# Performance work log

Hardware: AMD Instinct MI355X
Metric: run time of the kernel (lower is better)

Reference implementation:

```python
import jax, jax.numpy as jnp
import numpy as np

N, M, DIM, HEADS = 32768, 2048, 128, 8
TAU = 0.1


def setup_inputs() -> dict:
    key = jax.random.key(0)
    ks = jax.random.split(key, 7)
    return {
        "x1": jax.random.normal(ks[0], (N, DIM), jnp.float32),
        "k": jax.random.normal(ks[1], (N, DIM), jnp.float32),
        "c": jax.random.normal(ks[2], (M, DIM), jnp.float32),
        "Wq": jax.random.normal(ks[3], (DIM * HEADS, DIM), jnp.float32) * 0.02,
        "bq": jax.random.normal(ks[4], (DIM * HEADS,), jnp.float32) * 0.02,
        "Wd": jax.random.normal(ks[5], (DIM, DIM), jnp.float32) * 0.02,
        "bd": jax.random.normal(ks[6], (DIM,), jnp.float32) * 0.02,
    }


def reference(x1, k, c, Wq, bq, Wd, bd):
    # q and k both go through the same 'query' projection (as in the source)
    q = x1 @ Wq.T + bq                      # [N, dim*H]
    kq = k @ Wq.T + bq                      # [N, dim*H]
    C = jnp.tile(c, (1, HEADS))             # torch.cat([c]*H, dim=1) -> [M, dim*H]
    t = q + kq                              # additive attention 'scores' input
    logits = (t @ C.T) / jnp.sqrt(jnp.asarray(DIM, t.dtype))  # [N, M]
    p = jax.nn.softmax(logits, axis=-1)
    # gumbel_softmax(p, tau=0.1, hard=True): -log(Exp(1)) ~ Gumbel(0,1)
    noise = jax.random.gumbel(jax.random.key(42), p.shape, p.dtype)
    y_soft = jax.nn.softmax((p + noise) / TAU, axis=-1)
    idx = jnp.argmax(y_soft, axis=-1)
    y_hard = jax.nn.one_hot(idx, M, dtype=p.dtype)
    y = y_hard - jax.lax.stop_gradient(y_soft) + y_soft  # straight-through
    # attention_dropout and dropout are rate 0.0 -> identity
    out = y.T @ x1                          # [M, dim]
    return out @ Wd.T + bd                  # dense
```

## Files before the change

### kernel.cpp

```cpp
#include <hip/hip_runtime.h>
#include <stdint.h>
#include <math.h>

#define NROW 32768
#define MCOL 2048
#define KDIM 128
#define NHEAD 8
#define SCALE 0.08838834764831845f

typedef __attribute__((ext_vector_type(8))) short short8;
typedef __attribute__((ext_vector_type(4))) float f32x4;

__device__ __forceinline__ uint32_t rotl32(uint32_t x, uint32_t r) {
  return __builtin_amdgcn_alignbit(x, x, 32u - r);
}

__device__ __forceinline__ uint32_t tf_hash(uint32_t c) {
  const uint32_t K2 = 0x1BD11BDAu ^ 0u ^ 42u;
  uint32_t x0 = 0u, x1 = c + 42u;
#define R4A { x0 += x1; x1 = rotl32(x1,13); x1 ^= x0; \
              x0 += x1; x1 = rotl32(x1,15); x1 ^= x0; \
              x0 += x1; x1 = rotl32(x1,26); x1 ^= x0; \
              x0 += x1; x1 = rotl32(x1, 6); x1 ^= x0; }
#define R4B { x0 += x1; x1 = rotl32(x1,17); x1 ^= x0; \
              x0 += x1; x1 = rotl32(x1,29); x1 ^= x0; \
              x0 += x1; x1 = rotl32(x1,16); x1 ^= x0; \
              x0 += x1; x1 = rotl32(x1,24); x1 ^= x0; }
  R4A x0 += 42u;      x1 += K2 + 1u;
  R4B x0 += K2;       x1 += 2u;
  R4A    x1 += 42u + 3u;
  R4B x0 += 42u;      x1 += K2 + 4u;
  R4A x0 += K2;       x1 += 5u;
#undef R4A
#undef R4B
  return x0 ^ x1;
}

__device__ __forceinline__ float bits_to_u(uint32_t b) {
  uint32_t fb = (b >> 9) | 0x3F800000u;
  float f = __uint_as_float(fb) - 1.0f;
  return (f == 0.0f) ? 1.17549435e-38f : f;
}

__device__ __forceinline__ float gumbel_of_key(uint32_t key) {
  float u = bits_to_u(key);
  return -logf(-logf(u));
}

__global__ void k_wsum(const float* __restrict__ Wq, const float* __restrict__ bq,
                       float* __restrict__ Wsum, float* __restrict__ bsum) {
  int t = blockIdx.x * 256 + threadIdx.x;
  if (t < KDIM * KDIM) {
    int d = t >> 7, e = t & 127;
    float s = 0.f;
#pragma unroll
    for (int h = 0; h < NHEAD; ++h) s += Wq[(h * KDIM + d) * KDIM + e];
    Wsum[t] = s;
  }
  if (blockIdx.x == 0 && threadIdx.x < KDIM) {
    int d = threadIdx.x;
    float s = 0.f;
#pragma unroll
    for (int h = 0; h < NHEAD; ++h) s += bq[h * KDIM + d];
    bsum[d] = 2.0f * s;
  }
}

__global__ void k_cw(const float* __restrict__ c, const float* __restrict__ Wsum,
                     const float* __restrict__ bsum,
                     float* __restrict__ cw_s, unsigned short* __restrict__ cwB16,
                     float* __restrict__ cb_s) {
  int m = blockIdx.x;
  int e = threadIdx.x;
  __shared__ float crow[KDIM];
  if (e < 32) ((float4*)crow)[e] = ((const float4*)(c + (size_t)m * KDIM))[e];
  __syncthreads();
  float s = 0.f;
#pragma unroll 4
  for (int d = 0; d < KDIM; ++d) s += crow[d] * Wsum[d * KDIM + e];
  float sv = s * SCALE;
  cw_s[(size_t)m * KDIM + e] = sv;
  {
    int t = m >> 4, col = m & 15, ks = e >> 5, grp = (e >> 3) & 3, j = e & 7;
    int lane = grp * 16 + col;
    cwB16[(((size_t)(t * 4 + ks)) * 64 + lane) * 8 + j] =
        (unsigned short)(__float_as_uint(sv) >> 16);
  }
  if (e == 0) {
    float sb = 0.f;
    for (int d = 0; d < KDIM; ++d) sb += bsum[d] * crow[d];
    cb_s[m] = sb * SCALE;
  }
}

__launch_bounds__(256, 4)
__global__ void k_mega(const float* __restrict__ x1, const float* __restrict__ kin,
                       const uint4* __restrict__ cwB, const float* __restrict__ cb_s,
                       const float* __restrict__ cw_s, float* __restrict__ accum) {
  __shared__ float smx[32];
  __shared__ float sD[32];
  __shared__ float xksh[4][KDIM];

  const int tid = threadIdx.x;
  const int wv = tid >> 6, lane = tid & 63;
  const int B = blockIdx.x * 32;
  const int sstart = wv * 8;

  if (wv < 2) {
    const int R = B + wv * 16;
    const int rowA = R + (lane & 15);
    const int kbase = (lane >> 4) * 8;

    union { uint32_t u[4]; short8 s; } af[4];
#pragma unroll
    for (int ks = 0; ks < 4; ++ks) {
      const float* xp = x1 + (size_t)rowA * KDIM + ks * 32 + kbase;
      const float* kp = kin + (size_t)rowA * KDIM + ks * 32 + kbase;
      float4 a0 = *(const float4*)xp, a1 = *(const float4*)(xp + 4);
      float4 b0 = *(const float4*)kp, b1 = *(const float4*)(kp + 4);
      float f[8] = {a0.x + b0.x, a0.y + b0.y, a0.z + b0.z, a0.w + b0.w,
                    a1.x + b1.x, a1.y + b1.y, a1.z + b1.z, a1.w + b1.w};
#pragma unroll
      for (int r = 0; r < 4; ++r)
        af[ks].u[r] = (__float_as_uint(f[2 * r]) >> 16) |
                      (__float_as_uint(f[2 * r + 1]) & 0xFFFF0000u);
    }

    float mxs[4], Ds[4];
#pragma unroll
    for (int r = 0; r < 4; ++r) { mxs[r] = -INFINITY; Ds[r] = 0.f; }

#pragma unroll 2
    for (int t = 0; t < 128; ++t) {
      f32x4 acc = {0.f, 0.f, 0.f, 0.f};
#pragma unroll
      for (int ks = 0; ks < 4; ++ks) {
        union { uint4 v; short8 s; } bf;
        bf.v = cwB[(size_t)(t * 4 + ks) * 64 + lane];
        acc = __builtin_amdgcn_mfma_f32_16x16x32_bf16(af[ks].s, bf.s, acc, 0, 0, 0);
      }
      float cbv = cb_s[t * 16 + (lane & 15)];
#pragma unroll
      for (int r = 0; r < 4; ++r) {
        float lv = acc[r] + cbv;
        mxs[r] = fmaxf(mxs[r], lv);
        Ds[r] += __expf(lv);
      }
    }

#pragma unroll
    for (int s = 1; s < 16; s <<= 1) {
#pragma unroll
      for (int r = 0; r < 4; ++r) {
        mxs[r] = fmaxf(mxs[r], __shfl_xor(mxs[r], s));
        Ds[r] += __shfl_xor(Ds[r], s);
      }
    }
    if ((lane & 15) == 0) {
#pragma unroll
      for (int r = 0; r < 4; ++r) {
        int lr = wv * 16 + (lane >> 4) * 4 + r;
        smx[lr] = mxs[r];
        sD[lr] = Ds[r];
      }
    }
  }

  uint32_t tk0[8], tk1[8], tk2[8];
#pragma unroll
  for (int ri = 0; ri < 8; ++ri) {
    const int n = B + sstart + ri;
    const uint32_t c0 = (uint32_t)n * (uint32_t)MCOL + (uint32_t)lane;
    uint32_t t0 = 0u, t1 = 0u, t2 = 0u;
#pragma unroll 8
    for (uint32_t jj = 0; jj < 32; ++jj) {
      uint32_t b = tf_hash(c0 + 64u * jj);
      uint32_t key = (b & 0xFFFFFE00u) | jj;
      t2 = max(t2, min(min(t0, t1), key));
      t1 = max(t1, min(t0, key));
      t0 = max(t0, key);
    }
    tk0[ri] = t0; tk1[ri] = t1; tk2[ri] = t2;
  }

  __syncthreads();

#pragma unroll 1
  for (int ri = 0; ri < 8; ++ri) {
    const int n = B + sstart + ri;
    const int lr = sstart + ri;

    uint32_t t0 = tk0[ri], t1 = tk1[ri], t2 = tk2[ri];
    uint32_t kmax = t0;
#pragma unroll
    for (int s = 1; s < 64; s <<= 1)
      kmax = max(kmax, (uint32_t)__shfl_xor((int)kmax, s));

    const float mx = smx[lr], Dp = sD[lr];
    const float pmax = __expf(mx) / Dp;
    const float gstar = gumbel_of_key(kmax);
    const float thr = gstar - (pmax * 1.05f + 2e-4f);

    const float2 xa = ((const float2*)(x1 + (size_t)n * KDIM))[lane];
    const float2 xb = ((const float2*)(kin + (size_t)n * KDIM))[lane];
    const float xk0 = xa.x + xb.x, xk1 = xa.y + xb.y;

    float bestSc = -INFINITY;
    int bestM = 0x7FFFFFFF;

    if (pmax > 0.2f) {
      xksh[wv][lane * 2] = xk0;
      xksh[wv][lane * 2 + 1] = xk1;
      __builtin_amdgcn_s_waitcnt(0);
      for (uint32_t jj = 0; jj < 32; ++jj) {
        uint32_t m = (uint32_t)lane | (jj << 6);
        uint32_t b = tf_hash((uint32_t)n * (uint32_t)MCOL + m);
        float g = -logf(-logf(bits_to_u(b)));
        float l = 0.f;
        for (int e = 0; e < KDIM; ++e) l += xksh[wv][e] * cw_s[(size_t)m * KDIM + e];
        float p = __expf(l + cb_s[m]) / Dp;
        float sc = p + g;
        if (sc > bestSc || (sc == bestSc && (int)m < bestM)) { bestSc = sc; bestM = (int)m; }
      }
#pragma unroll
      for (int s = 1; s < 64; s <<= 1) {
        float os = __shfl_xor(bestSc, s);
        int om = __shfl_xor(bestM, s);
        if (os > bestSc || (os == bestSc && om < bestM)) { bestSc = os; bestM = om; }
      }
    } else {
#pragma unroll
      for (int s = 0; s < 3; ++s) {
        uint32_t tkv = (s == 0) ? t0 : ((s == 1) ? t1 : t2);
        float g = gumbel_of_key(tkv);
        unsigned long long bl = __ballot(g >= thr);
        while (bl) {
          int src = __ffsll(bl) - 1;
          bl &= bl - 1ull;
          uint32_t kk = (uint32_t)__shfl((int)tkv, src);
          float gc = __shfl(g, src);
          int m = src | (int)((kk & 31u) << 6);
          const float2 cv = ((const float2*)(cw_s + (size_t)m * KDIM))[lane];
          float part = xk0 * cv.x + xk1 * cv.y;
#pragma unroll
          for (int sh = 1; sh < 64; sh <<= 1) part += __shfl_xor(part, sh);
          float p = __expf(part + cb_s[m]) / Dp;
          float sc = p + gc;
          if (sc > bestSc || (sc == bestSc && m < bestM)) { bestSc = sc; bestM = m; }
        }
      }
    }

    float* dst = accum + (size_t)bestM * KDIM + lane * 2;
    atomicAdd(dst + 0, xa.x);
    atomicAdd(dst + 1, xa.y);
  }
}

__global__ void k_final(const float* __restrict__ acc, const float* __restrict__ Wd,
                        const float* __restrict__ bd, float* __restrict__ out) {
  int m = blockIdx.x, j = threadIdx.x;
  __shared__ float ar[KDIM];
  if (j < 32) ((float4*)ar)[j] = ((const float4*)(acc + (size_t)m * KDIM))[j];
  __syncthreads();
  const float4* wr = (const float4*)(Wd + (size_t)j * KDIM);
  float s = 0.f;
#pragma unroll
  for (int e4 = 0; e4 < 32; ++e4) {
    float4 wv = wr[e4];
    s += wv.x * ar[4 * e4 + 0] + wv.y * ar[4 * e4 + 1]
       + wv.z * ar[4 * e4 + 2] + wv.w * ar[4 * e4 + 3];
  }
  out[(size_t)m * KDIM + j] = s + bd[j];
}

extern "C" void kernel_launch(void* const* d_in, const int* in_sizes, int n_in,
                              void* d_out, int out_size, void* d_ws, size_t ws_size,
                              hipStream_t stream) {
  const float* x1 = (const float*)d_in[0];
  const float* k  = (const float*)d_in[1];
  const float* c  = (const float*)d_in[2];
  const float* Wq = (const float*)d_in[3];
  const float* bq = (const float*)d_in[4];
  const float* Wd = (const float*)d_in[5];
  const float* bd = (const float*)d_in[6];
  float* out = (float*)d_out;

  char* ws = (char*)d_ws;
  size_t off = 0;
  float* cw_s = (float*)(ws + off); off += (size_t)MCOL * KDIM * 4;
  float* cb_s = (float*)(ws + off); off += 8192;
  unsigned short* cwB = (unsigned short*)(ws + off); off += (size_t)MCOL * KDIM * 2;
  float* Wsum = (float*)(ws + off); off += KDIM * KDIM * 4;
  float* bsum = (float*)(ws + off); off += 4096;
  float* accum = (float*)(ws + off); off += (size_t)MCOL * KDIM * 4;

  hipMemsetAsync(accum, 0, (size_t)MCOL * KDIM * sizeof(float), stream);
  k_wsum<<<64, 256, 0, stream>>>(Wq, bq, Wsum, bsum);
  k_cw<<<MCOL, 128, 0, stream>>>(c, Wsum, bsum, cw_s, cwB, cb_s);
  k_mega<<<1024, 256, 0, stream>>>(x1, k, (const uint4*)cwB, cb_s, cw_s, accum);
  k_final<<<MCOL, 128, 0, stream>>>(accum, Wd, bd, out);
}
```

Baseline: 204.6 us.

## Collect high-Gumbel candidates via ballot compaction and rebalance rows across waves

Drops the per-lane top-3 key tracking. The kernel now compacts every hash above a fixed Gumbel threshold into a per-row shared-memory candidate list using a ballot and prefix popcount. The fast path then scans only those candidates, and it is proven safe when the threshold Gumbel lies below the best candidate minus the probability margin. Otherwise it falls back to the full scan. Rows are split 7/7/9/9 so the MFMA waves do less hashing, and the accum memset is folded into k_wsum. The tradeoff is extra shared memory and ballot traffic in the hash loop, plus a possible rise in fallbacks if candidate counts overflow or the threshold check fails.

```diff
diff --git a/kernel.cpp b/kernel.cpp
--- a/kernel.cpp
+++ b/kernel.cpp
@@ -7,6 +7,7 @@
 #define KDIM 128
 #define NHEAD 8
 #define SCALE 0.08838834764831845f
+#define CSLOTS 24
 
 typedef __attribute__((ext_vector_type(8))) short short8;
 typedef __attribute__((ext_vector_type(4))) float f32x4;
@@ -48,7 +49,8 @@
 }
 
 __global__ void k_wsum(const float* __restrict__ Wq, const float* __restrict__ bq,
-                       float* __restrict__ Wsum, float* __restrict__ bsum) {
+                       float* __restrict__ Wsum, float* __restrict__ bsum,
+                       float* __restrict__ accum) {
   int t = blockIdx.x * 256 + threadIdx.x;
   if (t < KDIM * KDIM) {
     int d = t >> 7, e = t & 127;
@@ -56,6 +58,12 @@
 #pragma unroll
     for (int h = 0; h < NHEAD; ++h) s += Wq[(h * KDIM + d) * KDIM + e];
     Wsum[t] = s;
+  }
+  {
+    float4 z = {0.f, 0.f, 0.f, 0.f};
+    float4* a4 = (float4*)accum;
+#pragma unroll
+    for (int r = 0; r < 4; ++r) a4[t + r * 16384] = z;
   }
   if (blockIdx.x == 0 && threadIdx.x < KDIM) {
     int d = threadIdx.x;
@@ -99,12 +107,17 @@
                        const float* __restrict__ cw_s, float* __restrict__ accum) {
   __shared__ float smx[32];
   __shared__ float sD[32];
+  __shared__ uint2 cls[4][9][CSLOTS];
   __shared__ float xksh[4][KDIM];
 
   const int tid = threadIdx.x;
   const int wv = tid >> 6, lane = tid & 63;
   const int B = blockIdx.x * 32;
-  const int sstart = wv * 8;
+  const int sstart = (wv < 2) ? wv * 7 : 14 + (wv - 2) * 9;
+  const int scnt = (wv < 2) ? 7 : 9;
+
+  const uint32_t BTHR = (__float_as_uint(1.0f + 0.996f) & 0x007FFFFFu) << 9;
+  const float GT = gumbel_of_key(BTHR);
 
   if (wv < 2) {
     const int R = B + wv * 16;
@@ -166,40 +179,40 @@
     }
   }
 
-  uint32_t tk0[8], tk1[8], tk2[8];
-#pragma unroll
-  for (int ri = 0; ri < 8; ++ri) {
-    const int n = B + sstart + ri;
-    const uint32_t c0 = (uint32_t)n * (uint32_t)MCOL + (uint32_t)lane;
-    uint32_t t0 = 0u, t1 = 0u, t2 = 0u;
+  uint32_t rcnt[9];
+#pragma unroll
+  for (int ri = 0; ri < 9; ++ri) {
+    if (ri < scnt) {
+      const int n = B + sstart + ri;
+      const uint32_t c0 = (uint32_t)n * (uint32_t)MCOL + (uint32_t)lane;
+      uint32_t cnt = 0u;
 #pragma unroll 8
-    for (uint32_t jj = 0; jj < 32; ++jj) {
-      uint32_t b = tf_hash(c0 + 64u * jj);
-      uint32_t key = (b & 0xFFFFFE00u) | jj;
-      t2 = max(t2, min(min(t0, t1), key));
-      t1 = max(t1, min(t0, key));
-      t0 = max(t0, key);
-    }
-    tk0[ri] = t0; tk1[ri] = t1; tk2[ri] = t2;
+      for (uint32_t jj = 0; jj < 32; ++jj) {
+        uint32_t b = tf_hash(c0 + 64u * jj);
+        unsigned long long mk = __ballot(b >= BTHR);
+        if (mk) {
+          uint32_t pos = cnt + (uint32_t)__popcll(mk & ((1ull << lane) - 1ull));
+          if (b >= BTHR && pos < CSLOTS)
+            cls[wv][ri][pos] = make_uint2(b, (uint32_t)lane | (jj << 6));
+          cnt += (uint32_t)__popcll(mk);
+        }
+      }
+      rcnt[ri] = cnt;
+    }
   }
 
   __syncthreads();
 
 #pragma unroll 1
-  for (int ri = 0; ri < 8; ++ri) {
-    const int n = B + sstart + ri;
+  for (int ri = 0; ri < 9; ++ri) {
+    if (ri >= scnt) break;
     const int lr = sstart + ri;
-
-    uint32_t t0 = tk0[ri], t1 = tk1[ri], t2 = tk2[ri];
-    uint32_t kmax = t0;
-#pragma unroll
-    for (int s = 1; s < 64; s <<= 1)
-      kmax = max(kmax, (uint32_t)__shfl_xor((int)kmax, s));
+    const int n = B + lr;
+    const uint32_t cnt = rcnt[ri];
 
     const float mx = smx[lr], Dp = sD[lr];
     const float pmax = __expf(mx) / Dp;
-    const float gstar = gumbel_of_key(kmax);
-    const float thr = gstar - (pmax * 1.05f + 2e-4f);
+    const float delta = pmax * 1.05f + 2e-4f;
 
     const float2 xa = ((const float2*)(x1 + (size_t)n * KDIM))[lane];
     const float2 xb = ((const float2*)(kin + (size_t)n * KDIM))[lane];
@@ -208,7 +221,18 @@
     float bestSc = -INFINITY;
     int bestM = 0x7FFFFFFF;
 
-    if (pmax > 0.2f) {
+    uint2 cd = make_uint2(0u, 0u);
+    if (lane < cnt && lane < CSLOTS) cd = cls[wv][ri][lane];
+    uint32_t kmax = cd.x;
+#pragma unroll
+    for (int s = 1; s < 64; s <<= 1)
+      kmax = max(kmax, (uint32_t)__shfl_xor((int)kmax, s));
+    const float gstar = gumbel_of_key(kmax);
+
+    const bool safe = (cnt >= 1u) && (cnt <= CSLOTS) && (pmax <= 0.2f) &&
+                      (GT <= gstar - delta);
+
+    if (!safe) {
       xksh[wv][lane * 2] = xk0;
       xksh[wv][lane * 2 + 1] = xk1;
       __builtin_amdgcn_s_waitcnt(0);
@@ -229,25 +253,21 @@
         if (os > bestSc || (os == bestSc && om < bestM)) { bestSc = os; bestM = om; }
       }
     } else {
-#pragma unroll
-      for (int s = 0; s < 3; ++s) {
-        uint32_t tkv = (s == 0) ? t0 : ((s == 1) ? t1 : t2);
-        float g = gumbel_of_key(tkv);
-        unsigned long long bl = __ballot(g >= thr);
-        while (bl) {
-          int src = __ffsll(bl) - 1;
-          bl &= bl - 1ull;
-          uint32_t kk = (uint32_t)__shfl((int)tkv, src);
-          float gc = __shfl(g, src);
-          int m = src | (int)((kk & 31u) << 6);
-          const float2 cv = ((const float2*)(cw_s + (size_t)m * KDIM))[lane];
-          float part = xk0 * cv.x + xk1 * cv.y;
-#pragma unroll
-          for (int sh = 1; sh < 64; sh <<= 1) part += __shfl_xor(part, sh);
-          float p = __expf(part + cb_s[m]) / Dp;
-          float sc = p + gc;
-          if (sc > bestSc || (sc == bestSc && m < bestM)) { bestSc = sc; bestM = m; }
-        }
+      float g = (lane < cnt) ? gumbel_of_key(cd.x) : -INFINITY;
+      const float thr = gstar - delta;
+      unsigned long long bl = __ballot(g >= thr);
+      while (bl) {
+        int src = __ffsll(bl) - 1;
+        bl &= bl - 1ull;
+        int m = __shfl((int)cd.y, src);
+        float gc = __shfl(g, src);
+        const float2 cv = ((const float2*)(cw_s + (size_t)m * KDIM))[lane];
+        float part = xk0 * cv.x + xk1 * cv.y;
+#pragma unroll
+        for (int sh = 1; sh < 64; sh <<= 1) part += __shfl_xor(part, sh);
+        float p = __expf(part + cb_s[m]) / Dp;
+        float sc = p + gc;
+        if (sc > bestSc || (sc == bestSc && m < bestM)) { bestSc = sc; bestM = m; }
       }
     }
 
@@ -295,8 +315,7 @@
   float* bsum = (float*)(ws + off); off += 4096;
   float* accum = (float*)(ws + off); off += (size_t)MCOL * KDIM * 4;
 
-  hipMemsetAsync(accum, 0, (size_t)MCOL * KDIM * sizeof(float), stream);
-  k_wsum<<<64, 256, 0, stream>>>(Wq, bq, Wsum, bsum);
+  k_wsum<<<64, 256, 0, stream>>>(Wq, bq, Wsum, bsum, accum);
   k_cw<<<MCOL, 128, 0, stream>>>(c, Wsum, bsum, cw_s, cwB, cb_s);
   k_mega<<<1024, 256, 0, stream>>>(x1, k, (const uint4*)cwB, cb_s, cw_s, accum);
   k_final<<<MCOL, 128, 0, stream>>>(accum, Wd, bd, out);
```

After: 307.0 us. 1.5x slower.

## Halve rows per block, split softmax-stat columns across rotating waves, fold memset

Applied to the files above, without the earlier changes.

Each block now handles 16 rows instead of 32 and the grid doubles. Two of the four waves, chosen by a role that rotates with the block index, each compute the softmax max and sum over half of the 2048 columns, and the partial results are merged through shared memory. The launch bound rises to 8 blocks per SM and the accumulator memset is folded into the Wsum kernel, removing one launch. The goal is to spread the MFMA statistics pass across waves to improve load balance and occupancy, at the cost of reading the A operand twice per row tile and higher register pressure under the tighter launch bound.

```diff
diff --git a/kernel.cpp b/kernel.cpp
--- a/kernel.cpp
+++ b/kernel.cpp
@@ -48,7 +48,8 @@
 }
 
 __global__ void k_wsum(const float* __restrict__ Wq, const float* __restrict__ bq,
-                       float* __restrict__ Wsum, float* __restrict__ bsum) {
+                       float* __restrict__ Wsum, float* __restrict__ bsum,
+                       float* __restrict__ accum) {
   int t = blockIdx.x * 256 + threadIdx.x;
   if (t < KDIM * KDIM) {
     int d = t >> 7, e = t & 127;
@@ -56,6 +57,12 @@
 #pragma unroll
     for (int h = 0; h < NHEAD; ++h) s += Wq[(h * KDIM + d) * KDIM + e];
     Wsum[t] = s;
+  }
+  {
+    float4 z = {0.f, 0.f, 0.f, 0.f};
+    float4* a4 = (float4*)accum;
+#pragma unroll
+    for (int r = 0; r < 4; ++r) a4[t + r * 16384] = z;
   }
   if (blockIdx.x == 0 && threadIdx.x < KDIM) {
     int d = threadIdx.x;
@@ -93,22 +100,22 @@
   }
 }
 
-__launch_bounds__(256, 4)
+__launch_bounds__(256, 8)
 __global__ void k_mega(const float* __restrict__ x1, const float* __restrict__ kin,
                        const uint4* __restrict__ cwB, const float* __restrict__ cb_s,
                        const float* __restrict__ cw_s, float* __restrict__ accum) {
-  __shared__ float smx[32];
-  __shared__ float sD[32];
+  __shared__ float smx_p[2][16];
+  __shared__ float sD_p[2][16];
   __shared__ float xksh[4][KDIM];
 
   const int tid = threadIdx.x;
   const int wv = tid >> 6, lane = tid & 63;
-  const int B = blockIdx.x * 32;
-  const int sstart = wv * 8;
-
-  if (wv < 2) {
-    const int R = B + wv * 16;
-    const int rowA = R + (lane & 15);
+  const int B = blockIdx.x * 16;
+  const int role = (wv + (int)blockIdx.x) & 3;
+  const int sstart = wv * 4;
+
+  if (role < 2) {
+    const int rowA = B + (lane & 15);
     const int kbase = (lane >> 4) * 8;
 
     union { uint32_t u[4]; short8 s; } af[4];
@@ -131,7 +138,8 @@
     for (int r = 0; r < 4; ++r) { mxs[r] = -INFINITY; Ds[r] = 0.f; }
 
 #pragma unroll 2
-    for (int t = 0; t < 128; ++t) {
+    for (int ti = 0; ti < 64; ++ti) {
+      const int t = role * 64 + ti;
       f32x4 acc = {0.f, 0.f, 0.f, 0.f};
 #pragma unroll
       for (int ks = 0; ks < 4; ++ks) {
@@ -159,16 +167,16 @@
     if ((lane & 15) == 0) {
 #pragma unroll
       for (int r = 0; r < 4; ++r) {
-        int lr = wv * 16 + (lane >> 4) * 4 + r;
-        smx[lr] = mxs[r];
-        sD[lr] = Ds[r];
-      }
-    }
-  }
-
-  uint32_t tk0[8], tk1[8], tk2[8];
-#pragma unroll
-  for (int ri = 0; ri < 8; ++ri) {
+        int lr = (lane >> 4) * 4 + r;
+        smx_p[role][lr] = mxs[r];
+        sD_p[role][lr] = Ds[r];
+      }
+    }
+  }
+
+  uint32_t tk0[4], tk1[4], tk2[4];
+#pragma unroll
+  for (int ri = 0; ri < 4; ++ri) {
     const int n = B + sstart + ri;
     const uint32_t c0 = (uint32_t)n * (uint32_t)MCOL + (uint32_t)lane;
     uint32_t t0 = 0u, t1 = 0u, t2 = 0u;
@@ -186,9 +194,9 @@
   __syncthreads();
 
 #pragma unroll 1
-  for (int ri = 0; ri < 8; ++ri) {
-    const int n = B + sstart + ri;
+  for (int ri = 0; ri < 4; ++ri) {
     const int lr = sstart + ri;
+    const int n = B + lr;
 
     uint32_t t0 = tk0[ri], t1 = tk1[ri], t2 = tk2[ri];
     uint32_t kmax = t0;
@@ -196,7 +204,8 @@
     for (int s = 1; s < 64; s <<= 1)
       kmax = max(kmax, (uint32_t)__shfl_xor((int)kmax, s));
 
-    const float mx = smx[lr], Dp = sD[lr];
+    const float mx = fmaxf(smx_p[0][lr], smx_p[1][lr]);
+    const float Dp = sD_p[0][lr] + sD_p[1][lr];
     const float pmax = __expf(mx) / Dp;
     const float gstar = gumbel_of_key(kmax);
     const float thr = gstar - (pmax * 1.05f + 2e-4f);
@@ -295,9 +304,8 @@
   float* bsum = (float*)(ws + off); off += 4096;
   float* accum = (float*)(ws + off); off += (size_t)MCOL * KDIM * 4;
 
-  hipMemsetAsync(accum, 0, (size_t)MCOL * KDIM * sizeof(float), stream);
-  k_wsum<<<64, 256, 0, stream>>>(Wq, bq, Wsum, bsum);
+  k_wsum<<<64, 256, 0, stream>>>(Wq, bq, Wsum, bsum, accum);
   k_cw<<<MCOL, 128, 0, stream>>>(c, Wsum, bsum, cw_s, cwB, cb_s);
-  k_mega<<<1024, 256, 0, stream>>>(x1, k, (const uint4*)cwB, cb_s, cw_s, accum);
+  k_mega<<<2048, 256, 0, stream>>>(x1, k, (const uint4*)cwB, cb_s, cw_s, accum);
   k_final<<<MCOL, 128, 0, stream>>>(accum, Wd, bd, out);
 }
```

Measured after the change: 225.4 us. +10.2%, slower.
